# Kernel tuning notes

Measured on AMD Instinct MI355X. Metric: run time of the kernel, lower is better.

The kernel has to match this reference:

```python
import jax, jax.numpy as jnp
import numpy as np

N, E, IN, H, C, L, K = 50000, 800000, 128, 96, 10, 4, 16
LN_EPS = 1e-5


def layer_norm(x, g, b):
    m = x.mean(-1, keepdims=True)
    v = ((x - m) ** 2).mean(-1, keepdims=True)
    return (x - m) * jax.lax.rsqrt(v + LN_EPS) * g + b


def gcn_conv(x, W, b, src, dst, n):
    # PyG GCNConv: add self-loops, symmetric normalization D^-1/2 (A+I) D^-1/2
    xw = x @ W  # [N, H]
    deg = jax.ops.segment_sum(jnp.ones(src.shape[0], x.dtype), dst, num_segments=n) + 1.0
    dinv = jax.lax.rsqrt(deg)  # [N]
    norm = dinv[src] * dinv[dst]  # [E]
    agg = jax.ops.segment_sum(xw[src] * norm[:, None], dst, num_segments=n)
    agg = agg + xw * (dinv * dinv)[:, None]  # self-loop contribution
    return agg + b


def pe_encode(eigvecs, eigvals, pe_eps, phi_w1, phi_w2, rho_w1, rho_b1, rho_w2, rho_b2):
    # eval mode: no random sign flip
    ev = eigvals + pe_eps  # [N, K]
    z = jnp.stack((eigvecs, ev), axis=2)  # [N, K, 2]
    z = jnp.nan_to_num(z)
    h = jax.nn.relu(z @ phi_w1) @ phi_w2  # [N, K, H]
    h = h.sum(axis=1)  # [N, H]
    return jax.nn.relu(h @ rho_w1 + rho_b1) @ rho_w2 + rho_b2


def setup_inputs() -> dict:
    key = jax.random.key(0)
    ks = jax.random.split(key, 24)
    s = 0.05
    inp = {
        "x": jax.random.normal(ks[0], (N, IN), jnp.float32),
        "edge_index": jax.random.randint(ks[1], (2, E), 0, N),
        "eigvecs": jax.random.normal(ks[2], (N, K), jnp.float32),
        "eigvals": jax.random.uniform(ks[3], (N, K), jnp.float32),
        "enc_W": jax.random.normal(ks[4], (IN, H), jnp.float32) * s,
        "enc_b": jnp.zeros((H,), jnp.float32),
        "in_g": jnp.ones((H,), jnp.float32),
        "in_b": jnp.zeros((H,), jnp.float32),
        "phi_w1": jax.random.normal(ks[5], (2, H), jnp.float32) * s,
        "phi_w2": jax.random.normal(ks[6], (H, H), jnp.float32) * s,
        "rho_w1": jax.random.normal(ks[7], (H, H), jnp.float32) * s,
        "rho_b1": jnp.zeros((H,), jnp.float32),
        "rho_w2": jax.random.normal(ks[8], (H, H), jnp.float32) * s,
        "rho_b2": jnp.zeros((H,), jnp.float32),
        "pe_eps": (1e-12 * jnp.arange(K, dtype=jnp.float32))[None],
        "conv_W": jax.random.normal(ks[9], (L, H, H), jnp.float32) * s,
        "conv_b": jnp.zeros((L, H), jnp.float32),
        "norm_g": jnp.ones((L, H), jnp.float32),
        "norm_b": jnp.zeros((L, H), jnp.float32),
        "head_w1": jax.random.normal(ks[10], (H, H), jnp.float32) * s,
        "head_b1": jnp.zeros((H,), jnp.float32),
        "head_g": jnp.ones((H,), jnp.float32),
        "head_b": jnp.zeros((H,), jnp.float32),
        "head_w2": jax.random.normal(ks[11], (H, C), jnp.float32) * s,
        "head_b2": jnp.zeros((C,), jnp.float32),
    }
    return inp


def reference(x, edge_index, eigvecs, eigvals, enc_W, enc_b, in_g, in_b,
              phi_w1, phi_w2, rho_w1, rho_b1, rho_w2, rho_b2, pe_eps,
              conv_W, conv_b, norm_g, norm_b,
              head_w1, head_b1, head_g, head_b, head_w2, head_b2):
    src, dst = edge_index[0], edge_index[1]
    h = layer_norm(x @ enc_W + enc_b, in_g, in_b)
    h = h + pe_encode(eigvecs, eigvals, pe_eps, phi_w1, phi_w2,
                      rho_w1, rho_b1, rho_w2, rho_b2)
    for l in range(L):
        c = gcn_conv(h, conv_W[l], conv_b[l], src, dst, N)
        u = layer_norm(jax.nn.gelu(c, approximate=False), norm_g[l], norm_b[l])
        h = h + u  # dropout p applied only in training; eval mode here
    z = layer_norm(jax.nn.gelu(h @ head_w1 + head_b1, approximate=False), head_g, head_b)
    return z @ head_w2 + head_b2
```

## Files before the change

kernel.cpp:

```cpp
#include <hip/hip_runtime.h>
#include <hip/hip_bf16.h>

#define N_NODES 50000
#define N_EDGES 800000
#define IN_DIM  128
#define H_DIM   96
#define C_DIM   10
#define L_LAYERS 4
#define K_EIG   16
#define LN_EPS_F 1e-5f

#define EPB 4096
#define NPB 196
#define BKT 512
#define NBK 98

typedef __attribute__((ext_vector_type(8))) short bf16x8;
typedef __attribute__((ext_vector_type(4))) float f32x4;


__device__ __forceinline__ float gelu_f(float x) {
    return 0.5f * x * (1.0f + erff(x * 0.7071067811865476f));
}

__device__ __forceinline__ ushort f2bf(float f) {
    union { float f; unsigned int u; } v; v.f = f;
    unsigned int r = v.u + 0x7fffu + ((v.u >> 16) & 1u);
    return (ushort)(r >> 16);
}

__device__ __forceinline__ float bflo(unsigned int v) { return __uint_as_float(v << 16); }
__device__ __forceinline__ float bfhi(unsigned int v) { return __uint_as_float(v & 0xffff0000u); }
__device__ __forceinline__ float bf2f(ushort u) { return __uint_as_float(((unsigned)u) << 16); }


__global__ void k_binA(const int* __restrict__ dst, int* __restrict__ cntmat) {
    __shared__ int hist[NBK];
    for (int i = threadIdx.x; i < NBK; i += 256) hist[i] = 0;
    __syncthreads();
    const int e0 = blockIdx.x * EPB;
    for (int i = threadIdx.x; i < EPB; i += 256) {
        int e = e0 + i;
        if (e < N_EDGES) atomicAdd(&hist[dst[e] >> 9], 1);
    }
    __syncthreads();
    for (int i = threadIdx.x; i < NBK; i += 256)
        cntmat[i * NPB + blockIdx.x] = hist[i];
}

__global__ void k_binB(int* __restrict__ cm, int n) {
    __shared__ int wsum[16];
    const int tid = threadIdx.x, lane = tid & 63, wid = tid >> 6;
    int carry = 0;
    for (int base = 0; base < n; base += 1024) {
        int i = base + tid;
        int v = (i < n) ? cm[i] : 0;
        int s = v;
#pragma unroll
        for (int off = 1; off < 64; off <<= 1) {
            int x = __shfl_up(s, off);
            if (lane >= off) s += x;
        }
        if (lane == 63) wsum[wid] = s;
        __syncthreads();
        if (tid < 64) {
            int ws = (lane < 16) ? wsum[lane] : 0;
#pragma unroll
            for (int off = 1; off < 16; off <<= 1) {
                int x = __shfl_up(ws, off);
                if (lane >= off) ws += x;
            }
            if (lane < 16) wsum[lane] = ws;
        }
        __syncthreads();
        int woff = (wid > 0) ? wsum[wid - 1] : 0;
        if (i < n) cm[i] = carry + woff + s - v;
        int tot = wsum[15];
        __syncthreads();
        carry += tot;
    }
    if (tid == 0) cm[n] = carry;
}

__global__ void k_binC(const int* __restrict__ src, const int* __restrict__ dst,
                       const int* __restrict__ offs, unsigned int* __restrict__ eb) {
    __shared__ int cur[NBK];
    for (int i = threadIdx.x; i < NBK; i += 256) cur[i] = offs[i * NPB + blockIdx.x];
    __syncthreads();
    const int e0 = blockIdx.x * EPB;
    for (int i = threadIdx.x; i < EPB; i += 256) {
        int e = e0 + i;
        if (e < N_EDGES) {
            int d = dst[e];
            int slot = atomicAdd(&cur[d >> 9], 1);
            eb[slot] = ((unsigned)(d & (BKT - 1)) << 16) | (unsigned)src[e];
        }
    }
}

__global__ void k_binD(const unsigned int* __restrict__ eb, const int* __restrict__ offs,
                       int* __restrict__ rowst, float* __restrict__ dinv,
                       int* __restrict__ csr) {
    __shared__ int cnt[BKT];
    __shared__ int wsum[16];
    const int b = blockIdx.x, t = threadIdx.x;
    const int ebeg = offs[b * NPB], eend = offs[(b + 1) * NPB];
    for (int i = t; i < BKT; i += 1024) cnt[i] = 0;
    __syncthreads();
    for (int i = ebeg + t; i < eend; i += 1024)
        atomicAdd(&cnt[eb[i] >> 16], 1);
    __syncthreads();
    const int lane = t & 63, wid = t >> 6;
    int v = 0, s = 0;
    if (t < BKT) {
        v = cnt[t]; s = v;
#pragma unroll
        for (int off = 1; off < 64; off <<= 1) {
            int x = __shfl_up(s, off);
            if (lane >= off) s += x;
        }
        if (lane == 63) wsum[wid] = s;
    }
    __syncthreads();
    if (t < 64) {
        int ws = (lane < 8) ? wsum[lane] : 0;
#pragma unroll
        for (int off = 1; off < 8; off <<= 1) {
            int x = __shfl_up(ws, off);
            if (lane >= off) ws += x;
        }
        if (lane < 8) wsum[lane] = ws;
    }
    __syncthreads();
    if (t < BKT) {
        int woff = (wid > 0) ? wsum[wid - 1] : 0;
        int excl = ebeg + woff + s - v;
        int row = b * BKT + t;
        if (row < N_NODES) {
            rowst[row] = excl;
            dinv[row] = rsqrtf((float)v + 1.0f);
        }
        cnt[t] = excl;
    }
    __syncthreads();
    for (int i = ebeg + t; i < eend; i += 1024) {
        unsigned e = eb[i];
        int p = atomicAdd(&cnt[e >> 16], 1);
        csr[p] = (int)(e & 0xFFFFu);
    }
    if (b == 0 && t == 0) rowst[N_NODES] = N_EDGES;
}


struct WSrc { const float* p[10]; };

__global__ void k_prep(WSrc ws, ushort* __restrict__ out) {
    int idx = blockIdx.x * 256 + threadIdx.x;
    if (idx < 12288) {
        int n = idx >> 7, k = idx & 127;
        out[idx] = f2bf(ws.p[0][k * 96 + n]);
    } else if (idx < 12288 + 8 * 9216) {
        int j = idx - 12288;
        int m = j / 9216, r = j - m * 9216;
        int n = r / 96, k = r - n * 96;
        out[idx] = f2bf(ws.p[m + 1][k * 96 + n]);
    } else if (idx < 12288 + 8 * 9216 + 1536) {
        int j = idx - 12288 - 8 * 9216;
        int c = j / 96, k = j - c * 96;
        out[idx] = (c < C_DIM) ? f2bf(ws.p[9][k * C_DIM + c]) : (ushort)0;
    }
}


template <int K_DIM, typename XT, int EPI>
__launch_bounds__(256)
__global__ void k_gemm(const XT* __restrict__ X, const ushort* __restrict__ Wt,
                       const float* __restrict__ bias, const float* __restrict__ g,
                       const float* __restrict__ beta, const float* __restrict__ dinvp,
                       const ushort* __restrict__ w2t, const float* __restrict__ b2,
                       void* __restrict__ outv) {
    constexpr int NK = K_DIM / 32;
    __shared__ ushort Tt[(EPI == 5) ? 4 * 16 * 104 : 4];
    const int lane = threadIdx.x & 63, wv = threadIdx.x >> 6;
    const int lrow = lane & 15, lk = (lane >> 4) * 8;
    const int grp = blockIdx.x * 4 + wv;
    if (grp >= N_NODES / 16) return;

    bf16x8 wf[6][NK];
#pragma unroll
    for (int nn = 0; nn < 6; ++nn)
#pragma unroll
        for (int kk = 0; kk < NK; ++kk)
            wf[nn][kk] = *(const bf16x8*)(&Wt[(size_t)(nn * 16 + lrow) * K_DIM + kk * 32 + lk]);

    bf16x8 af[NK];
    const int arow = grp * 16 + lrow;
    if constexpr (sizeof(XT) == 4) {
#pragma unroll
        for (int kk = 0; kk < NK; ++kk) {
            const float4* p = (const float4*)((const float*)X + (size_t)arow * K_DIM + kk * 32 + lk);
            float4 a = p[0], b = p[1];
            union { bf16x8 v; unsigned u[4]; } pk;
            pk.u[0] = (unsigned)f2bf(a.x) | ((unsigned)f2bf(a.y) << 16);
            pk.u[1] = (unsigned)f2bf(a.z) | ((unsigned)f2bf(a.w) << 16);
            pk.u[2] = (unsigned)f2bf(b.x) | ((unsigned)f2bf(b.y) << 16);
            pk.u[3] = (unsigned)f2bf(b.z) | ((unsigned)f2bf(b.w) << 16);
            af[kk] = pk.v;
        }
    } else {
#pragma unroll
        for (int kk = 0; kk < NK; ++kk)
            af[kk] = *(const bf16x8*)((const ushort*)X + (size_t)arow * K_DIM + kk * 32 + lk);
    }

    f32x4 acc[6];
#pragma unroll
    for (int nn = 0; nn < 6; ++nn) { acc[nn][0] = 0.f; acc[nn][1] = 0.f; acc[nn][2] = 0.f; acc[nn][3] = 0.f; }
#pragma unroll
    for (int nn = 0; nn < 6; ++nn)
#pragma unroll
        for (int kk = 0; kk < NK; ++kk)
            acc[nn] = __builtin_amdgcn_mfma_f32_16x16x32_bf16(af[kk], wf[nn][kk], acc[nn], 0, 0, 0);

    float bcol[6], gcol[6], ncol[6];
    if (EPI == 2 || EPI == 5) {
#pragma unroll
        for (int nn = 0; nn < 6; ++nn) {
            bcol[nn] = bias[nn * 16 + lrow];
            gcol[nn] = g[nn * 16 + lrow];
            ncol[nn] = beta[nn * 16 + lrow];
        }
    }

    ushort* tw = &Tt[(EPI == 5) ? wv * 16 * 104 : 0];
    const int rbase = grp * 16 + (lane >> 4) * 4;
#pragma unroll
    for (int reg = 0; reg < 4; ++reg) {
        const int row = rbase + reg;
        float v[6];
#pragma unroll
        for (int nn = 0; nn < 6; ++nn) {
            v[nn] = acc[nn][reg];
            if (EPI == 2 || EPI == 5) v[nn] += bcol[nn];
            if (EPI == 5) v[nn] = gelu_f(v[nn]);
        }
        if (EPI == 2 || EPI == 5) {
            float s = 0.f, s2 = 0.f;
#pragma unroll
            for (int nn = 0; nn < 6; ++nn) { s += v[nn]; s2 += v[nn] * v[nn]; }
#pragma unroll
            for (int off = 1; off < 16; off <<= 1) { s += __shfl_xor(s, off); s2 += __shfl_xor(s2, off); }
            float mean = s * (1.f / 96.f);
            float var = s2 * (1.f / 96.f) - mean * mean;
            float rs = rsqrtf(var + LN_EPS_F);
#pragma unroll
            for (int nn = 0; nn < 6; ++nn) v[nn] = (v[nn] - mean) * rs * gcol[nn] + ncol[nn];
        }
        if constexpr (EPI == 5) {
            const int rl = (lane >> 4) * 4 + reg;
#pragma unroll
            for (int nn = 0; nn < 6; ++nn)
                tw[rl * 104 + nn * 16 + lrow] = f2bf(v[nn]);
        } else if constexpr (EPI == 0) {
            float dvr = dinvp[row];
#pragma unroll
            for (int nn = 0; nn < 6; ++nn)
                ((ushort*)outv)[(size_t)row * 96 + nn * 16 + lrow] = f2bf(v[nn] * dvr);
        } else {
#pragma unroll
            for (int nn = 0; nn < 6; ++nn)
                ((ushort*)outv)[(size_t)row * 96 + nn * 16 + lrow] = f2bf(v[nn]);
        }
    }

    if constexpr (EPI == 5) {
        asm volatile("s_waitcnt lgkmcnt(0)" ::: "memory");
        __builtin_amdgcn_sched_barrier(0);
        bf16x8 tf[3], w2f[3];
#pragma unroll
        for (int kk = 0; kk < 3; ++kk) {
            tf[kk]  = *(const bf16x8*)(&tw[lrow * 104 + kk * 32 + lk]);
            w2f[kk] = *(const bf16x8*)(&w2t[lrow * 96 + kk * 32 + lk]);
        }
        f32x4 acc2;
        acc2[0] = 0.f; acc2[1] = 0.f; acc2[2] = 0.f; acc2[3] = 0.f;
#pragma unroll
        for (int kk = 0; kk < 3; ++kk)
            acc2 = __builtin_amdgcn_mfma_f32_16x16x32_bf16(tf[kk], w2f[kk], acc2, 0, 0, 0);
        const int c = lane & 15;
        if (c < C_DIM) {
#pragma unroll
            for (int reg = 0; reg < 4; ++reg) {
                int nrow = grp * 16 + (lane >> 4) * 4 + reg;
                ((float*)outv)[(size_t)nrow * C_DIM + c] = acc2[reg] + b2[c];
            }
        }
    }
}


__launch_bounds__(256)
__global__ void k_pe(const float* __restrict__ eigvecs, const float* __restrict__ eigvals,
                     const float* __restrict__ pe_eps, const float* __restrict__ phi_w1,
                     const ushort* __restrict__ w_phi2, const ushort* __restrict__ w_rho1,
                     const ushort* __restrict__ w_rho2, const float* __restrict__ rho_b1,
                     const float* __restrict__ rho_b2, ushort* __restrict__ hb) {
    constexpr int KP = 104;
    __shared__ ushort WL[96 * KP];
    __shared__ ushort T[64 * KP];
    const int t = threadIdx.x;
    const int base = blockIdx.x * 64;

    for (int i = t; i < 96 * 12; i += 256) {
        int n = i / 12, kc = (i - n * 12) * 8;
        *(uint4*)(&WL[n * KP + kc]) = *(const uint4*)(&w_phi2[n * 96 + kc]);
    }
    {
        int r = t >> 2, jg = t & 3;
        int row = base + r;
        float s[24];
#pragma unroll
        for (int j = 0; j < 24; ++j) s[j] = 0.f;
        if (row < N_NODES) {
            float w0[24], w1v[24];
#pragma unroll
            for (int j = 0; j < 24; ++j) { w0[j] = phi_w1[jg * 24 + j]; w1v[j] = phi_w1[96 + jg * 24 + j]; }
            for (int k = 0; k < K_EIG; ++k) {
                float a = eigvecs[(size_t)row * K_EIG + k];
                float b = eigvals[(size_t)row * K_EIG + k] + pe_eps[k];
#pragma unroll
                for (int j = 0; j < 24; ++j) s[j] += fmaxf(fmaf(a, w0[j], b * w1v[j]), 0.f);
            }
        }
#pragma unroll
        for (int j = 0; j < 12; ++j) {
            unsigned pk = (unsigned)f2bf(s[2 * j]) | ((unsigned)f2bf(s[2 * j + 1]) << 16);
            *(unsigned*)(&T[r * KP + jg * 24 + 2 * j]) = pk;
        }
    }
    __syncthreads();

    const int lane = t & 63, w = t >> 6;
    const int lrow = lane & 15, lk = (lane >> 4) * 8;
    const int rsub = (lane >> 4) * 4;
    float bc2[6], bc3[6];
#pragma unroll
    for (int nn = 0; nn < 6; ++nn) { bc2[nn] = rho_b1[nn * 16 + lrow]; bc3[nn] = rho_b2[nn * 16 + lrow]; }

    f32x4 acc[6];

    {
        bf16x8 af[3];
#pragma unroll
        for (int kk = 0; kk < 3; ++kk) af[kk] = *(const bf16x8*)(&T[(w * 16 + lrow) * KP + kk * 32 + lk]);
#pragma unroll
        for (int nn = 0; nn < 6; ++nn) { acc[nn][0] = 0.f; acc[nn][1] = 0.f; acc[nn][2] = 0.f; acc[nn][3] = 0.f; }
#pragma unroll
        for (int nn = 0; nn < 6; ++nn)
#pragma unroll
            for (int kk = 0; kk < 3; ++kk)
                acc[nn] = __builtin_amdgcn_mfma_f32_16x16x32_bf16(
                    af[kk], *(const bf16x8*)(&WL[(nn * 16 + lrow) * KP + kk * 32 + lk]), acc[nn], 0, 0, 0);
        __syncthreads();
#pragma unroll
        for (int reg = 0; reg < 4; ++reg)
#pragma unroll
            for (int nn = 0; nn < 6; ++nn)
                T[(w * 16 + rsub + reg) * KP + nn * 16 + lrow] = f2bf(acc[nn][reg]);
        for (int i = t; i < 96 * 12; i += 256) {
            int n = i / 12, kc = (i - n * 12) * 8;
            *(uint4*)(&WL[n * KP + kc]) = *(const uint4*)(&w_rho1[n * 96 + kc]);
        }
        __syncthreads();
    }

    {
        bf16x8 af[3];
#pragma unroll
        for (int kk = 0; kk < 3; ++kk) af[kk] = *(const bf16x8*)(&T[(w * 16 + lrow) * KP + kk * 32 + lk]);
#pragma unroll
        for (int nn = 0; nn < 6; ++nn) { acc[nn][0] = 0.f; acc[nn][1] = 0.f; acc[nn][2] = 0.f; acc[nn][3] = 0.f; }
#pragma unroll
        for (int nn = 0; nn < 6; ++nn)
#pragma unroll
            for (int kk = 0; kk < 3; ++kk)
                acc[nn] = __builtin_amdgcn_mfma_f32_16x16x32_bf16(
                    af[kk], *(const bf16x8*)(&WL[(nn * 16 + lrow) * KP + kk * 32 + lk]), acc[nn], 0, 0, 0);
        __syncthreads();
#pragma unroll
        for (int reg = 0; reg < 4; ++reg)
#pragma unroll
            for (int nn = 0; nn < 6; ++nn)
                T[(w * 16 + rsub + reg) * KP + nn * 16 + lrow] = f2bf(fmaxf(acc[nn][reg] + bc2[nn], 0.f));
        for (int i = t; i < 96 * 12; i += 256) {
            int n = i / 12, kc = (i - n * 12) * 8;
            *(uint4*)(&WL[n * KP + kc]) = *(const uint4*)(&w_rho2[n * 96 + kc]);
        }
        __syncthreads();
    }

    {
        bf16x8 af[3];
#pragma unroll
        for (int kk = 0; kk < 3; ++kk) af[kk] = *(const bf16x8*)(&T[(w * 16 + lrow) * KP + kk * 32 + lk]);
#pragma unroll
        for (int nn = 0; nn < 6; ++nn) { acc[nn][0] = 0.f; acc[nn][1] = 0.f; acc[nn][2] = 0.f; acc[nn][3] = 0.f; }
#pragma unroll
        for (int nn = 0; nn < 6; ++nn)
#pragma unroll
            for (int kk = 0; kk < 3; ++kk)
                acc[nn] = __builtin_amdgcn_mfma_f32_16x16x32_bf16(
                    af[kk], *(const bf16x8*)(&WL[(nn * 16 + lrow) * KP + kk * 32 + lk]), acc[nn], 0, 0, 0);
#pragma unroll
        for (int reg = 0; reg < 4; ++reg) {
            int row = base + w * 16 + rsub + reg;
            if (row < N_NODES) {
#pragma unroll
                for (int nn = 0; nn < 6; ++nn) {
                    size_t idx = (size_t)row * 96 + nn * 16 + lrow;
                    float hv = bf2f(hb[idx]) + acc[nn][reg] + bc3[nn];
                    hb[idx] = f2bf(hv);
                }
            }
        }
    }
}


#define GA_EDGE(c) { uint3 gv = *(const uint3*)(&xw[(c) * 48 + f * 3]); \
    a[0] += bflo(gv.x); a[1] += bfhi(gv.x); \
    a[2] += bflo(gv.y); a[3] += bfhi(gv.y); \
    a[4] += bflo(gv.z); a[5] += bfhi(gv.z); }

__launch_bounds__(256)
__global__ void k_agg(const unsigned int* __restrict__ xw, const int* __restrict__ rowst,
                      const int* __restrict__ csr, const float* __restrict__ dinv,
                      const float* __restrict__ bias, const float* __restrict__ g,
                      const float* __restrict__ beta, ushort* __restrict__ hb) {
    const int lane = threadIdx.x & 63, wid = threadIdx.x >> 6;
    const int f = lane & 15;
    const int eg = lane >> 4;
    float bb[6], gg[6], be[6];
#pragma unroll
    for (int j = 0; j < 6; ++j) { bb[j] = bias[f * 6 + j]; gg[j] = g[f * 6 + j]; be[j] = beta[f * 6 + j]; }
    const int w = blockIdx.x * 4 + wid, stride = gridDim.x * 4;
    for (int base = w * 4; base < N_NODES; base += stride * 4) {
        const int row = base + eg;
        int rs = rowst[row], re = rowst[row + 1];
        float dv = dinv[row];
        uint3 sv = *(const uint3*)(&xw[row * 48 + f * 3]);
        float a[6];
        a[0] = bflo(sv.x); a[1] = bfhi(sv.x);
        a[2] = bflo(sv.y); a[3] = bfhi(sv.y);
        a[4] = bflo(sv.z); a[5] = bfhi(sv.z);
        int i = rs;
        for (; i + 7 < re; i += 8) {
            int c0 = csr[i], c1 = csr[i + 1], c2 = csr[i + 2], c3 = csr[i + 3];
            int c4 = csr[i + 4], c5 = csr[i + 5], c6 = csr[i + 6], c7 = csr[i + 7];
            GA_EDGE(c0); GA_EDGE(c1); GA_EDGE(c2); GA_EDGE(c3);
            GA_EDGE(c4); GA_EDGE(c5); GA_EDGE(c6); GA_EDGE(c7);
        }
        for (; i + 3 < re; i += 4) {
            int c0 = csr[i], c1 = csr[i + 1], c2 = csr[i + 2], c3 = csr[i + 3];
            GA_EDGE(c0); GA_EDGE(c1); GA_EDGE(c2); GA_EDGE(c3);
        }
        for (; i < re; ++i) {
            int c0 = csr[i];
            GA_EDGE(c0);
        }
        float s = 0.f, s2 = 0.f;
#pragma unroll
        for (int j = 0; j < 6; ++j) {
            a[j] = fmaf(a[j], dv, bb[j]);
            a[j] = gelu_f(a[j]);
            s += a[j]; s2 += a[j] * a[j];
        }
#pragma unroll
        for (int off = 1; off < 16; off <<= 1) { s += __shfl_xor(s, off); s2 += __shfl_xor(s2, off); }
        float mean = s * (1.f / 96.f);
        float var = s2 * (1.f / 96.f) - mean * mean;
        float rs_ = rsqrtf(var + LN_EPS_F);
        unsigned int* hbp = (unsigned int*)(hb + (size_t)row * 96 + f * 6);
        unsigned hv0 = hbp[0], hv1 = hbp[1], hv2 = hbp[2];
        float v0 = bflo(hv0) + (a[0] - mean) * rs_ * gg[0] + be[0];
        float v1 = bfhi(hv0) + (a[1] - mean) * rs_ * gg[1] + be[1];
        float v2 = bflo(hv1) + (a[2] - mean) * rs_ * gg[2] + be[2];
        float v3 = bfhi(hv1) + (a[3] - mean) * rs_ * gg[3] + be[3];
        float v4 = bflo(hv2) + (a[4] - mean) * rs_ * gg[4] + be[4];
        float v5 = bfhi(hv2) + (a[5] - mean) * rs_ * gg[5] + be[5];
        hbp[0] = (unsigned)f2bf(v0) | ((unsigned)f2bf(v1) << 16);
        hbp[1] = (unsigned)f2bf(v2) | ((unsigned)f2bf(v3) << 16);
        hbp[2] = (unsigned)f2bf(v4) | ((unsigned)f2bf(v5) << 16);
    }
}


extern "C" void kernel_launch(void* const* d_in, const int* in_sizes, int n_in,
                              void* d_out, int out_size, void* d_ws, size_t ws_size,
                              hipStream_t stream) {
    (void)in_sizes; (void)n_in; (void)out_size; (void)ws_size;
    const float* x       = (const float*)d_in[0];
    const int*   eidx    = (const int*)d_in[1];
    const float* eigvecs = (const float*)d_in[2];
    const float* eigvals = (const float*)d_in[3];
    const float* enc_W   = (const float*)d_in[4];
    const float* enc_b   = (const float*)d_in[5];
    const float* in_g    = (const float*)d_in[6];
    const float* in_b    = (const float*)d_in[7];
    const float* phi_w1  = (const float*)d_in[8];
    const float* phi_w2  = (const float*)d_in[9];
    const float* rho_w1  = (const float*)d_in[10];
    const float* rho_b1  = (const float*)d_in[11];
    const float* rho_w2  = (const float*)d_in[12];
    const float* rho_b2  = (const float*)d_in[13];
    const float* pe_eps  = (const float*)d_in[14];
    const float* conv_W  = (const float*)d_in[15];
    const float* conv_b  = (const float*)d_in[16];
    const float* norm_g  = (const float*)d_in[17];
    const float* norm_b  = (const float*)d_in[18];
    const float* head_w1 = (const float*)d_in[19];
    const float* head_b1 = (const float*)d_in[20];
    const float* head_g  = (const float*)d_in[21];
    const float* head_b  = (const float*)d_in[22];
    const float* head_w2 = (const float*)d_in[23];
    const float* head_b2 = (const float*)d_in[24];
    float* out = (float*)d_out;

    const int* src = eidx;
    const int* dst = eidx + N_EDGES;

    char* ws = (char*)d_ws;
    size_t off = 0;
    auto alloc = [&](size_t bytes) {
        void* p = ws + off;
        off += (bytes + 255) & ~(size_t)255;
        return p;
    };
    ushort*   hb    = (ushort*)alloc(sizeof(ushort) * (size_t)N_NODES * H_DIM);
    ushort*   bufA  = (ushort*)alloc(sizeof(ushort) * (size_t)N_NODES * H_DIM);
    ushort*   wbf   = (ushort*)alloc(sizeof(ushort) * (12288 + 8 * 9216 + 1536));
    int*      rowst = (int*)alloc(sizeof(int) * (N_NODES + 1));
    float*    dinv  = (float*)alloc(sizeof(float) * N_NODES);
    int*      csr   = (int*)alloc(sizeof(int) * N_EDGES);
    int*      cm    = (int*)alloc(sizeof(int) * (NBK * NPB + 1));
    unsigned* eb    = (unsigned*)bufA;

    const int gb = (N_NODES / 16 + 3) / 4;
    const int pb = (N_NODES + 63) / 64;
    const int prep_n = 12288 + 8 * 9216 + 1536;

    WSrc wsrc;
    wsrc.p[0] = enc_W; wsrc.p[1] = phi_w2; wsrc.p[2] = rho_w1; wsrc.p[3] = rho_w2;
    for (int l = 0; l < 4; ++l) wsrc.p[4 + l] = conv_W + (size_t)l * 9216;
    wsrc.p[8] = head_w1; wsrc.p[9] = head_w2;
    k_prep<<<(prep_n + 255) / 256, 256, 0, stream>>>(wsrc, wbf);

    k_binA<<<NPB, 256, 0, stream>>>(dst, cm);
    k_binB<<<1, 1024, 0, stream>>>(cm, NBK * NPB);
    k_binC<<<NPB, 256, 0, stream>>>(src, dst, cm, eb);
    k_binD<<<NBK, 1024, 0, stream>>>(eb, cm, rowst, dinv, csr);

    const ushort* w_enc  = wbf;
    const ushort* w_head = wbf + 12288 + 7 * 9216;
    const ushort* w_2t   = wbf + 12288 + 8 * 9216;

    k_gemm<IN_DIM, float, 2><<<gb, 256, 0, stream>>>(x, w_enc, enc_b, in_g, in_b,
                                                     nullptr, nullptr, nullptr, hb);

    k_pe<<<pb, 256, 0, stream>>>(eigvecs, eigvals, pe_eps, phi_w1,
                                 wbf + 12288, wbf + 12288 + 9216, wbf + 12288 + 2 * 9216,
                                 rho_b1, rho_b2, hb);

    for (int l = 0; l < L_LAYERS; ++l) {
        k_gemm<96, ushort, 0><<<gb, 256, 0, stream>>>(hb, wbf + 12288 + (size_t)(3 + l) * 9216,
                                                      nullptr, nullptr, nullptr, dinv,
                                                      nullptr, nullptr, bufA);
        k_agg<<<2048, 256, 0, stream>>>((const unsigned int*)bufA, rowst, csr, dinv,
                                        conv_b + (size_t)l * 96, norm_g + (size_t)l * 96,
                                        norm_b + (size_t)l * 96, hb);
    }

    k_gemm<96, ushort, 5><<<gb, 256, 0, stream>>>(hb, w_head, head_b1, head_g, head_b,
                                                  nullptr, w_2t, head_b2, out);
}
```

Baseline: 271.3 us.

## Fuse encoder GEMM+LayerNorm into PE kernel and deepen aggregation gather unroll

Merges the input encoder GEMM with its LayerNorm into the positional-encoding kernel. The encoder result stays in registers and is added to the PE output before a single bf16 write to hb, which removes one kernel launch and a read-modify-write of hb. The aggregation loop now batches 16 neighbor indices and their gathers before accumulating, exposing more memory-level parallelism. The aggregation grid also changes from 2048 to 1563 blocks. The fused kernel holds more registers live, which may lower occupancy.

```diff
diff --git a/kernel.cpp b/kernel.cpp
--- a/kernel.cpp
+++ b/kernel.cpp
@@ -31,7 +31,6 @@
 
 __device__ __forceinline__ float bflo(unsigned int v) { return __uint_as_float(v << 16); }
 __device__ __forceinline__ float bfhi(unsigned int v) { return __uint_as_float(v & 0xffff0000u); }
-__device__ __forceinline__ float bf2f(ushort u) { return __uint_as_float(((unsigned)u) << 16); }
 
 
 __global__ void k_binA(const int* __restrict__ dst, int* __restrict__ cntmat) {
@@ -195,23 +194,9 @@
 
     bf16x8 af[NK];
     const int arow = grp * 16 + lrow;
-    if constexpr (sizeof(XT) == 4) {
-#pragma unroll
-        for (int kk = 0; kk < NK; ++kk) {
-            const float4* p = (const float4*)((const float*)X + (size_t)arow * K_DIM + kk * 32 + lk);
-            float4 a = p[0], b = p[1];
-            union { bf16x8 v; unsigned u[4]; } pk;
-            pk.u[0] = (unsigned)f2bf(a.x) | ((unsigned)f2bf(a.y) << 16);
-            pk.u[1] = (unsigned)f2bf(a.z) | ((unsigned)f2bf(a.w) << 16);
-            pk.u[2] = (unsigned)f2bf(b.x) | ((unsigned)f2bf(b.y) << 16);
-            pk.u[3] = (unsigned)f2bf(b.z) | ((unsigned)f2bf(b.w) << 16);
-            af[kk] = pk.v;
-        }
-    } else {
-#pragma unroll
-        for (int kk = 0; kk < NK; ++kk)
-            af[kk] = *(const bf16x8*)((const ushort*)X + (size_t)arow * K_DIM + kk * 32 + lk);
-    }
+#pragma unroll
+    for (int kk = 0; kk < NK; ++kk)
+        af[kk] = *(const bf16x8*)((const ushort*)X + (size_t)arow * K_DIM + kk * 32 + lk);
 
     f32x4 acc[6];
 #pragma unroll
@@ -223,7 +208,7 @@
             acc[nn] = __builtin_amdgcn_mfma_f32_16x16x32_bf16(af[kk], wf[nn][kk], acc[nn], 0, 0, 0);
 
     float bcol[6], gcol[6], ncol[6];
-    if (EPI == 2 || EPI == 5) {
+    if (EPI == 5) {
 #pragma unroll
         for (int nn = 0; nn < 6; ++nn) {
             bcol[nn] = bias[nn * 16 + lrow];
@@ -241,10 +226,9 @@
 #pragma unroll
         for (int nn = 0; nn < 6; ++nn) {
             v[nn] = acc[nn][reg];
-            if (EPI == 2 || EPI == 5) v[nn] += bcol[nn];
-            if (EPI == 5) v[nn] = gelu_f(v[nn]);
-        }
-        if (EPI == 2 || EPI == 5) {
+            if (EPI == 5) v[nn] = gelu_f(v[nn] + bcol[nn]);
+        }
+        if (EPI == 5) {
             float s = 0.f, s2 = 0.f;
 #pragma unroll
             for (int nn = 0; nn < 6; ++nn) { s += v[nn]; s2 += v[nn] * v[nn]; }
@@ -261,15 +245,11 @@
 #pragma unroll
             for (int nn = 0; nn < 6; ++nn)
                 tw[rl * 104 + nn * 16 + lrow] = f2bf(v[nn]);
-        } else if constexpr (EPI == 0) {
+        } else {
             float dvr = dinvp[row];
 #pragma unroll
             for (int nn = 0; nn < 6; ++nn)
                 ((ushort*)outv)[(size_t)row * 96 + nn * 16 + lrow] = f2bf(v[nn] * dvr);
-        } else {
-#pragma unroll
-            for (int nn = 0; nn < 6; ++nn)
-                ((ushort*)outv)[(size_t)row * 96 + nn * 16 + lrow] = f2bf(v[nn]);
         }
     }
 
@@ -300,16 +280,82 @@
 
 
 __launch_bounds__(256)
-__global__ void k_pe(const float* __restrict__ eigvecs, const float* __restrict__ eigvals,
-                     const float* __restrict__ pe_eps, const float* __restrict__ phi_w1,
-                     const ushort* __restrict__ w_phi2, const ushort* __restrict__ w_rho1,
-                     const ushort* __restrict__ w_rho2, const float* __restrict__ rho_b1,
-                     const float* __restrict__ rho_b2, ushort* __restrict__ hb) {
+__global__ void k_encpe(const float* __restrict__ x, const ushort* __restrict__ w_enc,
+                        const float* __restrict__ enc_b, const float* __restrict__ in_g,
+                        const float* __restrict__ in_b,
+                        const float* __restrict__ eigvecs, const float* __restrict__ eigvals,
+                        const float* __restrict__ pe_eps, const float* __restrict__ phi_w1,
+                        const ushort* __restrict__ w_phi2, const ushort* __restrict__ w_rho1,
+                        const ushort* __restrict__ w_rho2, const float* __restrict__ rho_b1,
+                        const float* __restrict__ rho_b2, ushort* __restrict__ hb) {
     constexpr int KP = 104;
     __shared__ ushort WL[96 * KP];
     __shared__ ushort T[64 * KP];
     const int t = threadIdx.x;
     const int base = blockIdx.x * 64;
+    const int lane = t & 63, w = t >> 6;
+    const int lrow = lane & 15, lk = (lane >> 4) * 8;
+    const int rsub = (lane >> 4) * 4;
+
+    float facc[6][4];
+    {
+        bf16x8 ewf[6][4];
+#pragma unroll
+        for (int nn = 0; nn < 6; ++nn)
+#pragma unroll
+            for (int kk = 0; kk < 4; ++kk)
+                ewf[nn][kk] = *(const bf16x8*)(&w_enc[(size_t)(nn * 16 + lrow) * IN_DIM + kk * 32 + lk]);
+        bf16x8 eaf[4];
+        const int arow = base + w * 16 + lrow;
+        if (arow < N_NODES) {
+#pragma unroll
+            for (int kk = 0; kk < 4; ++kk) {
+                const float4* p = (const float4*)(x + (size_t)arow * IN_DIM + kk * 32 + lk);
+                float4 aa = p[0], bb = p[1];
+                union { bf16x8 v; unsigned u[4]; } pk;
+                pk.u[0] = (unsigned)f2bf(aa.x) | ((unsigned)f2bf(aa.y) << 16);
+                pk.u[1] = (unsigned)f2bf(aa.z) | ((unsigned)f2bf(aa.w) << 16);
+                pk.u[2] = (unsigned)f2bf(bb.x) | ((unsigned)f2bf(bb.y) << 16);
+                pk.u[3] = (unsigned)f2bf(bb.z) | ((unsigned)f2bf(bb.w) << 16);
+                eaf[kk] = pk.v;
+            }
+        } else {
+            union { bf16x8 v; unsigned u[4]; } z; z.u[0] = z.u[1] = z.u[2] = z.u[3] = 0u;
+#pragma unroll
+            for (int kk = 0; kk < 4; ++kk) eaf[kk] = z.v;
+        }
+        f32x4 ea[6];
+#pragma unroll
+        for (int nn = 0; nn < 6; ++nn) { ea[nn][0] = 0.f; ea[nn][1] = 0.f; ea[nn][2] = 0.f; ea[nn][3] = 0.f; }
+#pragma unroll
+        for (int nn = 0; nn < 6; ++nn)
+#pragma unroll
+            for (int kk = 0; kk < 4; ++kk)
+                ea[nn] = __builtin_amdgcn_mfma_f32_16x16x32_bf16(eaf[kk], ewf[nn][kk], ea[nn], 0, 0, 0);
+        float eb_[6], eg_[6], en_[6];
+#pragma unroll
+        for (int nn = 0; nn < 6; ++nn) {
+            eb_[nn] = enc_b[nn * 16 + lrow];
+            eg_[nn] = in_g[nn * 16 + lrow];
+            en_[nn] = in_b[nn * 16 + lrow];
+        }
+#pragma unroll
+        for (int reg = 0; reg < 4; ++reg) {
+            float v[6];
+#pragma unroll
+            for (int nn = 0; nn < 6; ++nn) v[nn] = ea[nn][reg] + eb_[nn];
+            float s = 0.f, s2 = 0.f;
+#pragma unroll
+            for (int nn = 0; nn < 6; ++nn) { s += v[nn]; s2 += v[nn] * v[nn]; }
+#pragma unroll
+            for (int off = 1; off < 16; off <<= 1) { s += __shfl_xor(s, off); s2 += __shfl_xor(s2, off); }
+            float mean = s * (1.f / 96.f);
+            float var = s2 * (1.f / 96.f) - mean * mean;
+            float rs = rsqrtf(var + LN_EPS_F);
+#pragma unroll
+            for (int nn = 0; nn < 6; ++nn) facc[nn][reg] = (v[nn] - mean) * rs * eg_[nn] + en_[nn];
+        }
+    }
 
     for (int i = t; i < 96 * 12; i += 256) {
         int n = i / 12, kc = (i - n * 12) * 8;
@@ -340,9 +386,6 @@
     }
     __syncthreads();
 
-    const int lane = t & 63, w = t >> 6;
-    const int lrow = lane & 15, lk = (lane >> 4) * 8;
-    const int rsub = (lane >> 4) * 4;
     float bc2[6], bc3[6];
 #pragma unroll
     for (int nn = 0; nn < 6; ++nn) { bc2[nn] = rho_b1[nn * 16 + lrow]; bc3[nn] = rho_b2[nn * 16 + lrow]; }
@@ -418,8 +461,7 @@
 #pragma unroll
                 for (int nn = 0; nn < 6; ++nn) {
                     size_t idx = (size_t)row * 96 + nn * 16 + lrow;
-                    float hv = bf2f(hb[idx]) + acc[nn][reg] + bc3[nn];
-                    hb[idx] = f2bf(hv);
+                    hb[idx] = f2bf(facc[nn][reg] + acc[nn][reg] + bc3[nn]);
                 }
             }
         }
@@ -454,11 +496,19 @@
         a[2] = bflo(sv.y); a[3] = bfhi(sv.y);
         a[4] = bflo(sv.z); a[5] = bfhi(sv.z);
         int i = rs;
-        for (; i + 7 < re; i += 8) {
-            int c0 = csr[i], c1 = csr[i + 1], c2 = csr[i + 2], c3 = csr[i + 3];
-            int c4 = csr[i + 4], c5 = csr[i + 5], c6 = csr[i + 6], c7 = csr[i + 7];
-            GA_EDGE(c0); GA_EDGE(c1); GA_EDGE(c2); GA_EDGE(c3);
-            GA_EDGE(c4); GA_EDGE(c5); GA_EDGE(c6); GA_EDGE(c7);
+        for (; i + 15 < re; i += 16) {
+            int c[16];
+#pragma unroll
+            for (int u = 0; u < 16; ++u) c[u] = csr[i + u];
+            uint3 vv[16];
+#pragma unroll
+            for (int u = 0; u < 16; ++u) vv[u] = *(const uint3*)(&xw[c[u] * 48 + f * 3]);
+#pragma unroll
+            for (int u = 0; u < 16; ++u) {
+                a[0] += bflo(vv[u].x); a[1] += bfhi(vv[u].x);
+                a[2] += bflo(vv[u].y); a[3] += bfhi(vv[u].y);
+                a[4] += bflo(vv[u].z); a[5] += bfhi(vv[u].z);
+            }
         }
         for (; i + 3 < re; i += 4) {
             int c0 = csr[i], c1 = csr[i + 1], c2 = csr[i + 2], c3 = csr[i + 3];
@@ -547,6 +597,7 @@
 
     const int gb = (N_NODES / 16 + 3) / 4;
     const int pb = (N_NODES + 63) / 64;
+    const int ab = 1563;
     const int prep_n = 12288 + 8 * 9216 + 1536;
 
     WSrc wsrc;
@@ -564,20 +615,18 @@
     const ushort* w_head = wbf + 12288 + 7 * 9216;
     const ushort* w_2t   = wbf + 12288 + 8 * 9216;
 
-    k_gemm<IN_DIM, float, 2><<<gb, 256, 0, stream>>>(x, w_enc, enc_b, in_g, in_b,
-                                                     nullptr, nullptr, nullptr, hb);
-
-    k_pe<<<pb, 256, 0, stream>>>(eigvecs, eigvals, pe_eps, phi_w1,
-                                 wbf + 12288, wbf + 12288 + 9216, wbf + 12288 + 2 * 9216,
-                                 rho_b1, rho_b2, hb);
+    k_encpe<<<pb, 256, 0, stream>>>(x, w_enc, enc_b, in_g, in_b,
+                                    eigvecs, eigvals, pe_eps, phi_w1,
+                                    wbf + 12288, wbf + 12288 + 9216, wbf + 12288 + 2 * 9216,
+                                    rho_b1, rho_b2, hb);
 
     for (int l = 0; l < L_LAYERS; ++l) {
         k_gemm<96, ushort, 0><<<gb, 256, 0, stream>>>(hb, wbf + 12288 + (size_t)(3 + l) * 9216,
                                                       nullptr, nullptr, nullptr, dinv,
                                                       nullptr, nullptr, bufA);
-        k_agg<<<2048, 256, 0, stream>>>((const unsigned int*)bufA, rowst, csr, dinv,
-                                        conv_b + (size_t)l * 96, norm_g + (size_t)l * 96,
-                                        norm_b + (size_t)l * 96, hb);
+        k_agg<<<ab, 256, 0, stream>>>((const unsigned int*)bufA, rowst, csr, dinv,
+                                      conv_b + (size_t)l * 96, norm_g + (size_t)l * 96,
+                                      norm_b + (size_t)l * 96, hb);
     }
 
     k_gemm<96, ushort, 5><<<gb, 256, 0, stream>>>(hb, w_head, head_b1, head_g, head_b,
```

Result: slower. 292.8 us (+7.9%).
